# Performance work log

Hardware: AMD Instinct MI355X
Metric: run time of the kernel (lower is better)

Reference implementation:

```python
import jax, jax.numpy as jnp
import numpy as np

B, N, K = 8, 2048, 20  # clouds, points per cloud, kNN neighbors
NUM_CLASSES = 40


def _mlp3(x, w1, b1, w2, b2, w3, b3):
    x = jax.nn.relu(x @ w1 + b1)
    x = jax.nn.relu(x @ w2 + b2)
    return jax.nn.relu(x @ w3 + b3)


def _dynamic_edge_conv(x, w1, b1, w2, b2, w3, b3):
    # x: [B, N, D]. Recompute kNN graph in feature space (per cloud),
    # build edge features [x_i, x_j - x_i], MLP, max-aggregate over neighbors.
    s = jnp.sum(x * x, axis=-1)  # [B, N]
    d2 = s[:, :, None] + s[:, None, :] - 2.0 * jnp.einsum('bnd,bmd->bnm', x, x)  # [B,N,N]
    _, idx = jax.lax.top_k(-d2, K)  # [B, N, K], includes self (dist 0), matching torch_cluster.knn(x, x)
    xj = jax.vmap(lambda xb, ib: xb[ib])(x, idx)  # gather neighbors [B, N, K, D]
    xi = jnp.broadcast_to(x[:, :, None, :], xj.shape)
    e = jnp.concatenate([xi, xj - xi], axis=-1)  # [B, N, K, 2D]
    h = _mlp3(e, w1, b1, w2, b2, w3, b3)  # [B, N, K, H]
    return jnp.max(h, axis=2)  # max aggregation -> [B, N, H]


def setup_inputs() -> dict:
    key = jax.random.key(0)
    ks = jax.random.split(key, 32)

    def w(k, shape):
        fan_in = shape[0]
        return (jax.random.normal(k, shape, dtype=jnp.float32) / np.sqrt(fan_in)).astype(jnp.float32)

    inp = {
        'pos': jax.random.normal(ks[0], (B * N, 3), dtype=jnp.float32),
        'batch': jnp.repeat(jnp.arange(B, dtype=jnp.int64), N),
        # conv1 MLP: 6 -> 64 -> 64 -> 64
        'c1w1': w(ks[1], (6, 64)),   'c1b1': jnp.zeros((64,), jnp.float32),
        'c1w2': w(ks[2], (64, 64)),  'c1b2': jnp.zeros((64,), jnp.float32),
        'c1w3': w(ks[3], (64, 64)),  'c1b3': jnp.zeros((64,), jnp.float32),
        # conv2 MLP: 128 -> 128 -> 128 -> 256
        'c2w1': w(ks[4], (128, 128)), 'c2b1': jnp.zeros((128,), jnp.float32),
        'c2w2': w(ks[5], (128, 128)), 'c2b2': jnp.zeros((128,), jnp.float32),
        'c2w3': w(ks[6], (128, 256)), 'c2b3': jnp.zeros((256,), jnp.float32),
        # classifier head
        'l0w': w(ks[7], (256, 512)),  'l0b': jnp.zeros((512,), jnp.float32),
        'l1w': w(ks[8], (512, 256)),  'l1b': jnp.zeros((256,), jnp.float32),
        'l2w': w(ks[9], (256, 256)),  'l2b': jnp.zeros((256,), jnp.float32),
        'l3w': w(ks[10], (256, NUM_CLASSES)), 'l3b': jnp.zeros((NUM_CLASSES,), jnp.float32),
    }
    return inp


def reference(pos, batch,
              c1w1, c1b1, c1w2, c1b2, c1w3, c1b3,
              c2w1, c2b1, c2w2, c2b2, c2w3, c2b3,
              l0w, l0b, l1w, l1b, l2w, l2b, l3w, l3b):
    # batch is a contiguous equal-size partition: reshape to [B, N, 3]
    x = pos.reshape(B, N, 3)
    x = _dynamic_edge_conv(x, c1w1, c1b1, c1w2, c1b2, c1w3, c1b3)   # [B, N, 64]
    x = _dynamic_edge_conv(x, c2w1, c2b1, c2w2, c2b2, c2w3, c2b3)   # [B, N, 256]
    x = jax.nn.relu(x @ l0w + l0b)                                   # [B, N, 512]
    x = jnp.max(x, axis=1)                                           # global_max_pool -> [B, 512]
    x = jax.nn.relu(x @ l1w + l1b)
    x = jax.nn.relu(x @ l2w + l2b)
    # dropout(p=0.5) is identity at inference
    x = x @ l3w + l3b
    return jax.nn.log_softmax(x, axis=-1)  # [B, NUM_CLASSES]
```

## Files before the change

### kernel.cpp

```cpp
#include <hip/hip_runtime.h>
#include <hip/hip_bf16.h>
#include <math.h>

#define BB 8
#define NN 2048
#define KK 20

typedef short bf16x8 __attribute__((ext_vector_type(8)));
typedef float f32x4 __attribute__((ext_vector_type(4)));

__device__ __forceinline__ unsigned short f2bf(float f) {
  unsigned u = __float_as_uint(f);
  u += 0x7FFFu + ((u >> 16) & 1u);
  return (unsigned short)(u >> 16);
}
__device__ __forceinline__ float bf2f(unsigned short h) {
  return __uint_as_float(((unsigned)h) << 16);
}

__device__ __forceinline__ void topk_insert(float d, int m, float (&bd)[KK], int (&bi)[KK],
                                            float& worst, int& wslot) {
  if (d < worst) {
#pragma unroll
    for (int j = 0; j < KK; ++j) {
      if (j == wslot) { bd[j] = d; bi[j] = m; }
    }
    float w = -INFINITY;
    int s = 0;
#pragma unroll
    for (int j = 0; j < KK; ++j) {
      if (bd[j] > w) { w = bd[j]; s = j; }
    }
    worst = w;
    wslot = s;
  }
}

__device__ __forceinline__ void sins20(float (&s)[KK], float d) {
#pragma unroll
  for (int q = 0; q < KK - 1; ++q) s[q] = fminf(s[q], fmaxf(s[q + 1], d));
  s[KK - 1] = fminf(s[KK - 1], d);
}

__device__ __forceinline__ float knn1_dist(float sn, float ssq,
                                           float x0, float x1, float x2,
                                           float y0, float y1, float y2) {
  const float dot = fmaf(x0, y0, fmaf(x1, y1, x2 * y2));
  return fmaf(-2.f, dot, sn + ssq);
}

__global__ __launch_bounds__(256) void knn1_part(const float* __restrict__ pos,
                                                 float* __restrict__ candd,
                                                 int* __restrict__ candi) {
  __shared__ float xs0[256], xs1[256], xs2[256], ss[256];
  const int bid = blockIdx.x;
  const int b = bid >> 6;
  const int nc = (bid >> 3) & 7;
  const int mc = bid & 7;
  const int t = threadIdx.x;
  const float* posb = pos + (size_t)b * NN * 3;
  {
    const int m = mc * 256 + t;
    const float a0 = posb[m * 3 + 0];
    const float a1 = posb[m * 3 + 1];
    const float a2 = posb[m * 3 + 2];
    xs0[t] = a0; xs1[t] = a1; xs2[t] = a2;
    ss[t] = a0 * a0 + a1 * a1 + a2 * a2;
  }
  __syncthreads();
  const int n = nc * 256 + t;
  const float xn0 = posb[n * 3 + 0];
  const float xn1 = posb[n * 3 + 1];
  const float xn2 = posb[n * 3 + 2];
  const float sn = xn0 * xn0 + xn1 * xn1 + xn2 * xn2;

  float s[KK];
#pragma unroll
  for (int q = 0; q < KK; ++q) s[q] = INFINITY;
  for (int lm = 0; lm < 256; lm += 8) {
    float dv[8];
#pragma unroll
    for (int u = 0; u < 8; ++u)
      dv[u] = knn1_dist(sn, ss[lm + u], xn0, xn1, xn2, xs0[lm + u], xs1[lm + u], xs2[lm + u]);
#pragma unroll
    for (int u = 0; u < 8; ++u) sins20(s, dv[u]);
  }
  const float tau = s[0];

  int cA = 0;
  for (int lm = 0; lm < 256; lm += 8) {
#pragma unroll
    for (int u = 0; u < 8; ++u) {
      const float d = knn1_dist(sn, ss[lm + u], xn0, xn1, xn2, xs0[lm + u], xs1[lm + u], xs2[lm + u]);
      cA += (d < tau) ? 1 : 0;
    }
  }

  int posA = 0, posB = cA;
  const int rbase = mc * 256;
  const size_t obase = ((size_t)(b * 8 + mc) * KK) * 2048 + n;
  for (int lm = 0; lm < 256; lm += 8) {
#pragma unroll
    for (int u = 0; u < 8; ++u) {
      const float d = knn1_dist(sn, ss[lm + u], xn0, xn1, xn2, xs0[lm + u], xs1[lm + u], xs2[lm + u]);
      if (d < tau) {
        candd[obase + (size_t)posA * 2048] = d;
        candi[obase + (size_t)posA * 2048] = rbase + lm + u;
        ++posA;
      } else if (d == tau && posB < KK) {
        candd[obase + (size_t)posB * 2048] = d;
        candi[obase + (size_t)posB * 2048] = rbase + lm + u;
        ++posB;
      }
    }
  }
}

template <int NCH, int G>
__global__ __launch_bounds__(256) void merge_topk2(const float* __restrict__ candd,
                                                   const int* __restrict__ candi,
                                                   int* __restrict__ idx_out) {
  const int gid = blockIdx.x * 256 + threadIdx.x;
  const int pt = gid / G;
  const int sub = gid % G;
  const int b = pt >> 11, n = pt & 2047;
  constexpr int CPT = NCH / G;
  float bd[KK]; int bi[KK];
#pragma unroll
  for (int j = 0; j < KK; ++j) { bd[j] = INFINITY; bi[j] = 0; }
  float worst = INFINITY;
  int wslot = 0;
#pragma unroll
  for (int cc = 0; cc < CPT; ++cc) {
    const int c = sub * CPT + cc;
    const size_t base = ((size_t)(b * NCH + c) * KK) * 2048 + n;
    float dv[KK]; int iv[KK];
#pragma unroll
    for (int j = 0; j < KK; ++j) dv[j] = candd[base + (size_t)j * 2048];
#pragma unroll
    for (int j = 0; j < KK; ++j) iv[j] = candi[base + (size_t)j * 2048];
#pragma unroll
    for (int j = 0; j < KK; ++j) topk_insert(dv[j], iv[j], bd, bi, worst, wslot);
  }
#pragma unroll
  for (int stride = 1; stride < G; stride <<= 1) {
    float od[KK]; int oi[KK];
#pragma unroll
    for (int q = 0; q < KK; ++q) {
      od[q] = __shfl_xor(bd[q], stride);
      oi[q] = __shfl_xor(bi[q], stride);
    }
#pragma unroll
    for (int q = 0; q < KK; ++q) topk_insert(od[q], oi[q], bd, bi, worst, wslot);
  }
  if (sub == 0) {
    int* op = idx_out + (size_t)pt * KK;
#pragma unroll
    for (int j = 0; j < KK; ++j) op[j] = bi[j];
  }
}

__global__ __launch_bounds__(256) void pre1_kernel(const float* __restrict__ pos,
                                                   const float* __restrict__ w1,
                                                   const float* __restrict__ b1,
                                                   float* __restrict__ U1,
                                                   float* __restrict__ V1) {
  const int t = threadIdx.x;
  const int c = t & 63;
  const int n = blockIdx.x * 4 + (t >> 6);
  const float p0 = pos[(size_t)n * 3 + 0];
  const float p1 = pos[(size_t)n * 3 + 1];
  const float p2 = pos[(size_t)n * 3 + 2];
  const float wt0 = w1[0 * 64 + c], wt1 = w1[1 * 64 + c], wt2 = w1[2 * 64 + c];
  const float wb0 = w1[3 * 64 + c], wb1 = w1[4 * 64 + c], wb2 = w1[5 * 64 + c];
  float v = p0 * wb0 + p1 * wb1 + p2 * wb2;
  float u = p0 * (wt0 - wb0) + p1 * (wt1 - wb1) + p2 * (wt2 - wb2) + b1[c];
  U1[(size_t)n * 64 + c] = u;
  V1[(size_t)n * 64 + c] = v;
}

__global__ __launch_bounds__(256) void pre2_kernel(const float* __restrict__ x1,
                                                   const float* __restrict__ w1,
                                                   const float* __restrict__ b1,
                                                   float* __restrict__ U,
                                                   float* __restrict__ V) {
  __shared__ float X[64][68];
  const int nbase = blockIdx.x * 64;
  const int t = threadIdx.x;
  for (int it = t; it < 1024; it += 256) {
    const int r = it >> 4, q = it & 15;
    *(float4*)&X[r][q * 4] = *(const float4*)&x1[(size_t)(nbase + r) * 64 + q * 4];
  }
  __syncthreads();
  const int ty = t >> 4, tx = t & 15;
  const int c0 = tx * 8;
  float accT[4][8], accB[4][8];
#pragma unroll
  for (int u = 0; u < 4; ++u)
#pragma unroll
    for (int i = 0; i < 8; ++i) { accT[u][i] = 0.f; accB[u][i] = 0.f; }
  for (int d0 = 0; d0 < 64; d0 += 4) {
    float4 a[4];
#pragma unroll
    for (int u = 0; u < 4; ++u) a[u] = *(const float4*)&X[ty * 4 + u][d0];
#pragma unroll
    for (int dd = 0; dd < 4; ++dd) {
      const float4 t0 = *(const float4*)&w1[(size_t)(d0 + dd) * 128 + c0];
      const float4 t1 = *(const float4*)&w1[(size_t)(d0 + dd) * 128 + c0 + 4];
      const float4 bb0 = *(const float4*)&w1[(size_t)(64 + d0 + dd) * 128 + c0];
      const float4 bb1 = *(const float4*)&w1[(size_t)(64 + d0 + dd) * 128 + c0 + 4];
#pragma unroll
      for (int u = 0; u < 4; ++u) {
        const float av = (dd == 0) ? a[u].x : (dd == 1) ? a[u].y : (dd == 2) ? a[u].z : a[u].w;
        accT[u][0] = fmaf(av, t0.x, accT[u][0]);
        accT[u][1] = fmaf(av, t0.y, accT[u][1]);
        accT[u][2] = fmaf(av, t0.z, accT[u][2]);
        accT[u][3] = fmaf(av, t0.w, accT[u][3]);
        accT[u][4] = fmaf(av, t1.x, accT[u][4]);
        accT[u][5] = fmaf(av, t1.y, accT[u][5]);
        accT[u][6] = fmaf(av, t1.z, accT[u][6]);
        accT[u][7] = fmaf(av, t1.w, accT[u][7]);
        accB[u][0] = fmaf(av, bb0.x, accB[u][0]);
        accB[u][1] = fmaf(av, bb0.y, accB[u][1]);
        accB[u][2] = fmaf(av, bb0.z, accB[u][2]);
        accB[u][3] = fmaf(av, bb0.w, accB[u][3]);
        accB[u][4] = fmaf(av, bb1.x, accB[u][4]);
        accB[u][5] = fmaf(av, bb1.y, accB[u][5]);
        accB[u][6] = fmaf(av, bb1.z, accB[u][6]);
        accB[u][7] = fmaf(av, bb1.w, accB[u][7]);
      }
    }
  }
  const float4 bA = *(const float4*)&b1[c0];
  const float4 bB = *(const float4*)&b1[c0 + 4];
#pragma unroll
  for (int u = 0; u < 4; ++u) {
    const size_t row = (size_t)(nbase + ty * 4 + u) * 128 + c0;
    float4 u0, u1, v0, v1;
    v0 = make_float4(accB[u][0], accB[u][1], accB[u][2], accB[u][3]);
    v1 = make_float4(accB[u][4], accB[u][5], accB[u][6], accB[u][7]);
    u0.x = accT[u][0] - accB[u][0] + bA.x;
    u0.y = accT[u][1] - accB[u][1] + bA.y;
    u0.z = accT[u][2] - accB[u][2] + bA.z;
    u0.w = accT[u][3] - accB[u][3] + bA.w;
    u1.x = accT[u][4] - accB[u][4] + bB.x;
    u1.y = accT[u][5] - accB[u][5] + bB.y;
    u1.z = accT[u][6] - accB[u][6] + bB.z;
    u1.w = accT[u][7] - accB[u][7] + bB.w;
    *(float4*)&U[row] = u0;
    *(float4*)&U[row + 4] = u1;
    *(float4*)&V[row] = v0;
    *(float4*)&V[row + 4] = v1;
  }
}

__global__ __launch_bounds__(256) void wprep_kernel(
    const float* __restrict__ c2w2, const float* __restrict__ c2w3,
    const float* __restrict__ c1w2, const float* __restrict__ c1w3,
    unsigned short* __restrict__ w2t, unsigned short* __restrict__ w3t,
    unsigned short* __restrict__ c1w2hi, unsigned short* __restrict__ c1w2lo,
    unsigned short* __restrict__ c1w3hi, unsigned short* __restrict__ c1w3lo) {
  const int i = blockIdx.x * 256 + threadIdx.x;
  if (i < 16384) {
    const int d = i >> 7, c = i & 127;
    w2t[c * 128 + d] = f2bf(c2w2[i]);
  } else if (i < 49152) {
    const int j = i - 16384;
    const int d = j >> 8, c = j & 255;
    w3t[c * 128 + d] = f2bf(c2w3[j]);
  } else if (i < 53248) {
    const int j = i - 49152;
    const int d = j >> 6, c = j & 63;
    const float v = c1w2[j];
    const unsigned short h = f2bf(v);
    c1w2hi[c * 64 + d] = h;
    c1w2lo[c * 64 + d] = f2bf(v - bf2f(h));
  } else {
    const int j = i - 53248;
    const int d = j >> 6, c = j & 63;
    const float v = c1w3[j];
    const unsigned short h = f2bf(v);
    c1w3hi[c * 64 + d] = h;
    c1w3lo[c * 64 + d] = f2bf(v - bf2f(h));
  }
}

__global__ __launch_bounds__(256) void conv1_kernel(
    const float* __restrict__ U1, const float* __restrict__ V1,
    const int* __restrict__ idx,
    const unsigned short* __restrict__ w2hi, const unsigned short* __restrict__ w2lo,
    const float* __restrict__ b2,
    const unsigned short* __restrict__ w3hi, const unsigned short* __restrict__ w3lo,
    const float* __restrict__ b3,
    float* __restrict__ xout) {
  __shared__ __align__(16) unsigned short A[160][2][76];
  __shared__ unsigned int pm[8][64];
  const int bid = blockIdx.x;
  const int b = bid >> 8;
  const int pbase = (bid & 255) * 8;
  const int t = threadIdx.x;
  const int wave = t >> 6, lane = t & 63;
  const int lrow = lane & 15;
  const int lk8 = (lane >> 4) * 8;
  const int c = wave * 16 + lrow;

  for (int it = t; it < 2560; it += 256) {
    const int r = it >> 4, q = it & 15;
    const int p = r / 20, k = r - (r / 20) * 20;
    const int n = b * NN + pbase + p;
    const int j = b * NN + idx[(size_t)n * KK + k];
    const float4 uv = *(const float4*)&U1[(size_t)n * 64 + q * 4];
    const float4 vv = *(const float4*)&V1[(size_t)j * 64 + q * 4];
    float e[4];
    e[0] = fmaxf(uv.x + vv.x, 0.f);
    e[1] = fmaxf(uv.y + vv.y, 0.f);
    e[2] = fmaxf(uv.z + vv.z, 0.f);
    e[3] = fmaxf(uv.w + vv.w, 0.f);
    ushort4 hi, lo;
    hi.x = f2bf(e[0]); lo.x = f2bf(e[0] - bf2f(hi.x));
    hi.y = f2bf(e[1]); lo.y = f2bf(e[1] - bf2f(hi.y));
    hi.z = f2bf(e[2]); lo.z = f2bf(e[2] - bf2f(hi.z));
    hi.w = f2bf(e[3]); lo.w = f2bf(e[3] - bf2f(hi.w));
    *(ushort4*)&A[r][0][q * 4] = hi;
    *(ushort4*)&A[r][1][q * 4] = lo;
  }
  for (int i = t; i < 512; i += 256) ((unsigned int*)pm)[i] = 0u;
  __syncthreads();

  {
    bf16x8 whi[2], wlo[2];
#pragma unroll
    for (int ks = 0; ks < 2; ++ks) {
      whi[ks] = *(const bf16x8*)&w2hi[(size_t)c * 64 + ks * 32 + lk8];
      wlo[ks] = *(const bf16x8*)&w2lo[(size_t)c * 64 + ks * 32 + lk8];
    }
    f32x4 acc2[10];
#pragma unroll
    for (int mt = 0; mt < 10; ++mt) {
      bf16x8 ahi[2], alo[2];
#pragma unroll
      for (int ks = 0; ks < 2; ++ks) {
        ahi[ks] = *(const bf16x8*)&A[mt * 16 + lrow][0][ks * 32 + lk8];
        alo[ks] = *(const bf16x8*)&A[mt * 16 + lrow][1][ks * 32 + lk8];
      }
      f32x4 acc = {0.f, 0.f, 0.f, 0.f};
#pragma unroll
      for (int ks = 0; ks < 2; ++ks) {
        acc = __builtin_amdgcn_mfma_f32_16x16x32_bf16(ahi[ks], whi[ks], acc, 0, 0, 0);
        acc = __builtin_amdgcn_mfma_f32_16x16x32_bf16(ahi[ks], wlo[ks], acc, 0, 0, 0);
        acc = __builtin_amdgcn_mfma_f32_16x16x32_bf16(alo[ks], whi[ks], acc, 0, 0, 0);
      }
      acc2[mt] = acc;
    }
    __syncthreads();
    const float bias = b2[c];
#pragma unroll
    for (int mt = 0; mt < 10; ++mt) {
      const int r0 = mt * 16 + ((lane >> 4) << 2);
#pragma unroll
      for (int reg = 0; reg < 4; ++reg) {
        const float v = fmaxf(acc2[mt][reg] + bias, 0.f);
        const unsigned short h = f2bf(v);
        A[r0 + reg][0][c] = h;
        A[r0 + reg][1][c] = f2bf(v - bf2f(h));
      }
    }
  }
  __syncthreads();

  {
    bf16x8 whi[2], wlo[2];
#pragma unroll
    for (int ks = 0; ks < 2; ++ks) {
      whi[ks] = *(const bf16x8*)&w3hi[(size_t)c * 64 + ks * 32 + lk8];
      wlo[ks] = *(const bf16x8*)&w3lo[(size_t)c * 64 + ks * 32 + lk8];
    }
    const float bias = b3[c];
#pragma unroll
    for (int mt = 0; mt < 10; ++mt) {
      bf16x8 ahi[2], alo[2];
#pragma unroll
      for (int ks = 0; ks < 2; ++ks) {
        ahi[ks] = *(const bf16x8*)&A[mt * 16 + lrow][0][ks * 32 + lk8];
        alo[ks] = *(const bf16x8*)&A[mt * 16 + lrow][1][ks * 32 + lk8];
      }
      f32x4 acc = {0.f, 0.f, 0.f, 0.f};
#pragma unroll
      for (int ks = 0; ks < 2; ++ks) {
        acc = __builtin_amdgcn_mfma_f32_16x16x32_bf16(ahi[ks], whi[ks], acc, 0, 0, 0);
        acc = __builtin_amdgcn_mfma_f32_16x16x32_bf16(ahi[ks], wlo[ks], acc, 0, 0, 0);
        acc = __builtin_amdgcn_mfma_f32_16x16x32_bf16(alo[ks], whi[ks], acc, 0, 0, 0);
      }
      const int r0 = mt * 16 + ((lane >> 4) << 2);
      const float v0 = fmaxf(acc[0] + bias, 0.f);
      const float v1 = fmaxf(acc[1] + bias, 0.f);
      const float v2 = fmaxf(acc[2] + bias, 0.f);
      const float v3 = fmaxf(acc[3] + bias, 0.f);
      if (r0 / 20 == (r0 + 3) / 20) {
        atomicMax(&pm[r0 / 20][c], __float_as_uint(fmaxf(fmaxf(v0, v1), fmaxf(v2, v3))));
      } else {
        atomicMax(&pm[(r0 + 0) / 20][c], __float_as_uint(v0));
        atomicMax(&pm[(r0 + 1) / 20][c], __float_as_uint(v1));
        atomicMax(&pm[(r0 + 2) / 20][c], __float_as_uint(v2));
        atomicMax(&pm[(r0 + 3) / 20][c], __float_as_uint(v3));
      }
    }
  }
  __syncthreads();

  {
    const int p = t >> 5;
    const int cc = (t & 31) * 2;
    float2 o;
    o.x = __uint_as_float(pm[p][cc]);
    o.y = __uint_as_float(pm[p][cc + 1]);
    *(float2*)&xout[((size_t)(b * NN + pbase + p)) * 64 + cc] = o;
  }
}

__global__ __launch_bounds__(256) void xsplit_kernel(const float* __restrict__ x1,
                                                     unsigned short* __restrict__ xhi,
                                                     unsigned short* __restrict__ xlo,
                                                     float* __restrict__ s) {
  const int e = blockIdx.x * 256 + threadIdx.x;
  const int n = e >> 3, q = e & 7;
  const float4 v0 = *(const float4*)&x1[(size_t)n * 64 + q * 8];
  const float4 v1 = *(const float4*)&x1[(size_t)n * 64 + q * 8 + 4];
  float ps = v0.x * v0.x + v0.y * v0.y + v0.z * v0.z + v0.w * v0.w +
             v1.x * v1.x + v1.y * v1.y + v1.z * v1.z + v1.w * v1.w;
  ps += __shfl_xor(ps, 1);
  ps += __shfl_xor(ps, 2);
  ps += __shfl_xor(ps, 4);
  if (q == 0) s[n] = ps;
  const float vv[8] = {v0.x, v0.y, v0.z, v0.w, v1.x, v1.y, v1.z, v1.w};
  unsigned short hb[8], lb[8];
#pragma unroll
  for (int i = 0; i < 8; ++i) {
    hb[i] = f2bf(vv[i]);
    lb[i] = f2bf(vv[i] - bf2f(hb[i]));
  }
  *(ushort4*)&xhi[(size_t)n * 64 + q * 8] = make_ushort4(hb[0], hb[1], hb[2], hb[3]);
  *(ushort4*)&xhi[(size_t)n * 64 + q * 8 + 4] = make_ushort4(hb[4], hb[5], hb[6], hb[7]);
  *(ushort4*)&xlo[(size_t)n * 64 + q * 8] = make_ushort4(lb[0], lb[1], lb[2], lb[3]);
  *(ushort4*)&xlo[(size_t)n * 64 + q * 8 + 4] = make_ushort4(lb[4], lb[5], lb[6], lb[7]);
}

__global__ __launch_bounds__(256) void d2sel_kernel(const unsigned short* __restrict__ xhi,
                                                    const unsigned short* __restrict__ xlo,
                                                    const float* __restrict__ s,
                                                    float* __restrict__ candd,
                                                    int* __restrict__ candi) {
  __shared__ __align__(16) unsigned short SBUF[4 * 128 * 72];
  __shared__ float sA[128], sB[128];
  float (*Tt)[132] = (float(*)[132])SBUF;
  const int bid = blockIdx.x;
  const int b = bid >> 8;
  const int tile = bid & 255;
  const int ti = tile >> 4, tj = tile & 15;
  const int i0 = ti * 128, j0 = tj * 128;
  const int gb = b * NN;
  const int t = threadIdx.x;
  const int wave = t >> 6, lane = t & 63;
  const int lrow = lane & 15;
  const int lk8 = (lane >> 4) * 8;

  for (int it = t; it < 4096; it += 256) {
    const int part = it >> 10;
    const int r = (it >> 3) & 127;
    const int g = it & 7;
    const unsigned short* src = (part == 0) ? xhi : (part == 1) ? xlo
                               : (part == 2) ? xhi : xlo;
    const int base = (part < 2) ? i0 : j0;
    *(uint4*)&SBUF[part * 9216 + r * 72 + g * 8] =
        *(const uint4*)&src[((size_t)(gb + base + r)) * 64 + g * 8];
  }
  if (t < 128) sA[t] = s[gb + i0 + t];
  else sB[t - 128] = s[gb + j0 + (t - 128)];
  __syncthreads();

  bf16x8 ahi[2][2], alo[2][2];
#pragma unroll
  for (int mt = 0; mt < 2; ++mt) {
    const int r = wave * 32 + mt * 16 + lrow;
#pragma unroll
    for (int ks = 0; ks < 2; ++ks) {
      ahi[mt][ks] = *(const bf16x8*)&SBUF[0 * 9216 + r * 72 + ks * 32 + lk8];
      alo[mt][ks] = *(const bf16x8*)&SBUF[1 * 9216 + r * 72 + ks * 32 + lk8];
    }
  }
  f32x4 acc[2][8];
#pragma unroll
  for (int mt = 0; mt < 2; ++mt)
#pragma unroll
    for (int nt = 0; nt < 8; ++nt) acc[mt][nt] = (f32x4){0.f, 0.f, 0.f, 0.f};
#pragma unroll
  for (int nt = 0; nt < 8; ++nt) {
    bf16x8 bhi[2], blo[2];
#pragma unroll
    for (int ks = 0; ks < 2; ++ks) {
      bhi[ks] = *(const bf16x8*)&SBUF[2 * 9216 + (nt * 16 + lrow) * 72 + ks * 32 + lk8];
      blo[ks] = *(const bf16x8*)&SBUF[3 * 9216 + (nt * 16 + lrow) * 72 + ks * 32 + lk8];
    }
#pragma unroll
    for (int mt = 0; mt < 2; ++mt) {
#pragma unroll
      for (int ks = 0; ks < 2; ++ks) {
        acc[mt][nt] = __builtin_amdgcn_mfma_f32_16x16x32_bf16(ahi[mt][ks], bhi[ks], acc[mt][nt], 0, 0, 0);
        acc[mt][nt] = __builtin_amdgcn_mfma_f32_16x16x32_bf16(ahi[mt][ks], blo[ks], acc[mt][nt], 0, 0, 0);
        acc[mt][nt] = __builtin_amdgcn_mfma_f32_16x16x32_bf16(alo[mt][ks], bhi[ks], acc[mt][nt], 0, 0, 0);
      }
    }
  }
  __syncthreads();

#pragma unroll
  for (int mt = 0; mt < 2; ++mt) {
    const int ib = wave * 32 + mt * 16 + ((lane >> 4) << 2);
#pragma unroll
    for (int nt = 0; nt < 8; ++nt) {
      const int jj = nt * 16 + lrow;
      const float sj = sB[jj];
      float4 o;
      o.x = sA[ib + 0] + sj - 2.f * acc[mt][nt][0];
      o.y = sA[ib + 1] + sj - 2.f * acc[mt][nt][1];
      o.z = sA[ib + 2] + sj - 2.f * acc[mt][nt][2];
      o.w = sA[ib + 3] + sj - 2.f * acc[mt][nt][3];
      *(float4*)&Tt[jj][ib] = o;
    }
  }
  __syncthreads();

  const int j = t >> 1, h = t & 1;
  float sl[KK];
#pragma unroll
  for (int q = 0; q < KK; ++q) sl[q] = INFINITY;
  for (int r4 = 0; r4 < 16; ++r4) {
    const float4 v = *(const float4*)&Tt[j][h * 64 + r4 * 4];
    sins20(sl, v.x);
    sins20(sl, v.y);
    sins20(sl, v.z);
    sins20(sl, v.w);
  }
  {
    float od[KK];
#pragma unroll
    for (int q = 0; q < KK; ++q) od[q] = __shfl_xor(sl[q], 1);
#pragma unroll
    for (int q = 0; q < KK; ++q) sins20(sl, od[q]);
  }
  const float tau = sl[0];

  int cA = 0, cB = 0;
  for (int r4 = 0; r4 < 16; ++r4) {
    const float4 v = *(const float4*)&Tt[j][h * 64 + r4 * 4];
    cA += (v.x < tau) + (v.y < tau) + (v.z < tau) + (v.w < tau);
    cB += (v.x == tau) + (v.y == tau) + (v.z == tau) + (v.w == tau);
  }
  const int pA = __shfl_xor(cA, 1);
  const int pB = __shfl_xor(cB, 1);
  const int nA = cA + pA;
  int posA = h ? pA : 0;
  int posB = nA + (h ? pB : 0);

  const size_t obase = ((size_t)(b * 16 + ti) * KK) * 2048 + (j0 + j);
  for (int r4 = 0; r4 < 16; ++r4) {
    const float4 v = *(const float4*)&Tt[j][h * 64 + r4 * 4];
    const float dd[4] = {v.x, v.y, v.z, v.w};
#pragma unroll
    for (int u = 0; u < 4; ++u) {
      const float d = dd[u];
      const int row = i0 + h * 64 + r4 * 4 + u;
      if (d < tau) {
        candd[obase + (size_t)posA * 2048] = d;
        candi[obase + (size_t)posA * 2048] = row;
        ++posA;
      } else if (d == tau && posB < KK) {
        candd[obase + (size_t)posB * 2048] = d;
        candi[obase + (size_t)posB * 2048] = row;
        ++posB;
      }
    }
  }
}

__global__ __launch_bounds__(256) void conv2_kernel(
    const float* __restrict__ U, const float* __restrict__ V,
    const int* __restrict__ idx,
    const unsigned short* __restrict__ w2t, const float* __restrict__ b2,
    const unsigned short* __restrict__ w3t, const float* __restrict__ b3,
    float* __restrict__ xout) {
  __shared__ __align__(16) unsigned short E[80][136];
  __shared__ __align__(16) unsigned short E2[80][136];
  __shared__ unsigned int pm[4][256];
  const int bid = blockIdx.x;
  const int b = bid >> 9;
  const int pbase = (bid & 511) * 4;
  const int t = threadIdx.x;
  const int wave = t >> 6, lane = t & 63;
  const int lrow = lane & 15;
  const int lk8 = (lane >> 4) * 8;

  for (int it = t; it < 2560; it += 256) {
    const int r = it >> 5, q = it & 31;
    const int p = r / 20, k = r - (r / 20) * 20;
    const int n = b * NN + pbase + p;
    const int j = b * NN + idx[(size_t)n * KK + k];
    const float4 uv = *(const float4*)&U[(size_t)n * 128 + q * 4];
    const float4 vv = *(const float4*)&V[(size_t)j * 128 + q * 4];
    ushort4 h;
    h.x = f2bf(fmaxf(uv.x + vv.x, 0.f));
    h.y = f2bf(fmaxf(uv.y + vv.y, 0.f));
    h.z = f2bf(fmaxf(uv.z + vv.z, 0.f));
    h.w = f2bf(fmaxf(uv.w + vv.w, 0.f));
    *(ushort4*)&E[r][q * 4] = h;
  }
  for (int i = t; i < 1024; i += 256) ((unsigned int*)pm)[i] = 0u;
  __syncthreads();

  {
    bf16x8 wf[2][4];
#pragma unroll
    for (int nt2 = 0; nt2 < 2; ++nt2) {
      const int ntg = wave * 2 + nt2;
#pragma unroll
      for (int ks = 0; ks < 4; ++ks)
        wf[nt2][ks] = *(const bf16x8*)&w2t[(size_t)(ntg * 16 + lrow) * 128 + ks * 32 + lk8];
    }
    const float bias0 = b2[wave * 32 + lrow];
    const float bias1 = b2[wave * 32 + 16 + lrow];
#pragma unroll
    for (int mt = 0; mt < 5; ++mt) {
      bf16x8 af[4];
#pragma unroll
      for (int ks = 0; ks < 4; ++ks)
        af[ks] = *(const bf16x8*)&E[mt * 16 + lrow][ks * 32 + lk8];
      f32x4 acc0 = {0.f, 0.f, 0.f, 0.f};
      f32x4 acc1 = {0.f, 0.f, 0.f, 0.f};
#pragma unroll
      for (int ks = 0; ks < 4; ++ks) {
        acc0 = __builtin_amdgcn_mfma_f32_16x16x32_bf16(af[ks], wf[0][ks], acc0, 0, 0, 0);
        acc1 = __builtin_amdgcn_mfma_f32_16x16x32_bf16(af[ks], wf[1][ks], acc1, 0, 0, 0);
      }
      const int r0 = mt * 16 + ((lane >> 4) << 2);
      const int c0 = wave * 32 + lrow;
#pragma unroll
      for (int reg = 0; reg < 4; ++reg) {
        E2[r0 + reg][c0]      = f2bf(fmaxf(acc0[reg] + bias0, 0.f));
        E2[r0 + reg][c0 + 16] = f2bf(fmaxf(acc1[reg] + bias1, 0.f));
      }
    }
  }
  __syncthreads();

  {
    bf16x8 wf[4][4];
#pragma unroll
    for (int nt4 = 0; nt4 < 4; ++nt4) {
      const int ntg = wave * 4 + nt4;
#pragma unroll
      for (int ks = 0; ks < 4; ++ks)
        wf[nt4][ks] = *(const bf16x8*)&w3t[(size_t)(ntg * 16 + lrow) * 128 + ks * 32 + lk8];
    }
#pragma unroll
    for (int mt = 0; mt < 5; ++mt) {
      bf16x8 af[4];
#pragma unroll
      for (int ks = 0; ks < 4; ++ks)
        af[ks] = *(const bf16x8*)&E2[mt * 16 + lrow][ks * 32 + lk8];
      f32x4 acc[4];
#pragma unroll
      for (int nt4 = 0; nt4 < 4; ++nt4) acc[nt4] = (f32x4){0.f, 0.f, 0.f, 0.f};
#pragma unroll
      for (int ks = 0; ks < 4; ++ks) {
#pragma unroll
        for (int nt4 = 0; nt4 < 4; ++nt4)
          acc[nt4] = __builtin_amdgcn_mfma_f32_16x16x32_bf16(af[ks], wf[nt4][ks], acc[nt4], 0, 0, 0);
      }
      const int r0 = mt * 16 + ((lane >> 4) << 2);
      const int pa = r0 / 20;
      const int pb = (r0 + 3) / 20;
#pragma unroll
      for (int nt4 = 0; nt4 < 4; ++nt4) {
        const int c = wave * 64 + nt4 * 16 + lrow;
        const float bias = b3[c];
        float v0 = fmaxf(acc[nt4][0] + bias, 0.f);
        float v1 = fmaxf(acc[nt4][1] + bias, 0.f);
        float v2 = fmaxf(acc[nt4][2] + bias, 0.f);
        float v3 = fmaxf(acc[nt4][3] + bias, 0.f);
        if (pa == pb) {
          atomicMax(&pm[pa][c], __float_as_uint(fmaxf(fmaxf(v0, v1), fmaxf(v2, v3))));
        } else {
          atomicMax(&pm[(r0 + 0) / 20][c], __float_as_uint(v0));
          atomicMax(&pm[(r0 + 1) / 20][c], __float_as_uint(v1));
          atomicMax(&pm[(r0 + 2) / 20][c], __float_as_uint(v2));
          atomicMax(&pm[(r0 + 3) / 20][c], __float_as_uint(v3));
        }
      }
    }
  }
  __syncthreads();

  {
    const int p = t >> 6;
    const int c0 = (t & 63) * 4;
    const float4 o = *(const float4*)&pm[p][c0];
    *(float4*)&xout[((size_t)b * NN + pbase + p) * 256 + c0] = o;
  }
}

__global__ __launch_bounds__(256) void l0_kernel(const float* __restrict__ x2,
                                                 const float* __restrict__ w,
                                                 const float* __restrict__ bias,
                                                 float* __restrict__ gp) {
  __shared__ float A[64][68];
  __shared__ float red[16][128];
  const int bid = blockIdx.x;
  const int b = bid >> 7;
  const int mblk = (bid >> 2) & 31;
  const int cblk = bid & 3;
  const int t = threadIdx.x;
  const int ty = t >> 4, tx = t & 15;
  const float* xb = x2 + ((size_t)b * NN + mblk * 64) * 256;
  float acc[4][8];
#pragma unroll
  for (int u = 0; u < 4; ++u)
#pragma unroll
    for (int i = 0; i < 8; ++i) acc[u][i] = 0.f;
  for (int kc = 0; kc < 4; ++kc) {
    {
      const int r = t >> 2, seg = (t & 3) * 16;
#pragma unroll
      for (int s4 = 0; s4 < 4; ++s4) {
        *(float4*)&A[r][seg + s4 * 4] =
            *(const float4*)&xb[(size_t)r * 256 + kc * 64 + seg + s4 * 4];
      }
    }
    __syncthreads();
    for (int d0 = 0; d0 < 64; d0 += 4) {
      float4 a[4];
#pragma unroll
      for (int u = 0; u < 4; ++u) a[u] = *(const float4*)&A[ty * 4 + u][d0];
#pragma unroll
      for (int dd = 0; dd < 4; ++dd) {
        const size_t wrow = (size_t)(kc * 64 + d0 + dd) * 512 + cblk * 128 + tx * 8;
        const float4 wA = *(const float4*)&w[wrow];
        const float4 wB = *(const float4*)&w[wrow + 4];
#pragma unroll
        for (int u = 0; u < 4; ++u) {
          const float av = (dd == 0) ? a[u].x : (dd == 1) ? a[u].y : (dd == 2) ? a[u].z : a[u].w;
          acc[u][0] = fmaf(av, wA.x, acc[u][0]);
          acc[u][1] = fmaf(av, wA.y, acc[u][1]);
          acc[u][2] = fmaf(av, wA.z, acc[u][2]);
          acc[u][3] = fmaf(av, wA.w, acc[u][3]);
          acc[u][4] = fmaf(av, wB.x, acc[u][4]);
          acc[u][5] = fmaf(av, wB.y, acc[u][5]);
          acc[u][6] = fmaf(av, wB.z, acc[u][6]);
          acc[u][7] = fmaf(av, wB.w, acc[u][7]);
        }
      }
    }
    __syncthreads();
  }
  {
    float4 m0, m1;
    m0.x = fmaxf(fmaxf(acc[0][0], acc[1][0]), fmaxf(acc[2][0], acc[3][0]));
    m0.y = fmaxf(fmaxf(acc[0][1], acc[1][1]), fmaxf(acc[2][1], acc[3][1]));
    m0.z = fmaxf(fmaxf(acc[0][2], acc[1][2]), fmaxf(acc[2][2], acc[3][2]));
    m0.w = fmaxf(fmaxf(acc[0][3], acc[1][3]), fmaxf(acc[2][3], acc[3][3]));
    m1.x = fmaxf(fmaxf(acc[0][4], acc[1][4]), fmaxf(acc[2][4], acc[3][4]));
    m1.y = fmaxf(fmaxf(acc[0][5], acc[1][5]), fmaxf(acc[2][5], acc[3][5]));
    m1.z = fmaxf(fmaxf(acc[0][6], acc[1][6]), fmaxf(acc[2][6], acc[3][6]));
    m1.w = fmaxf(fmaxf(acc[0][7], acc[1][7]), fmaxf(acc[2][7], acc[3][7]));
    *(float4*)&red[ty][tx * 8] = m0;
    *(float4*)&red[ty][tx * 8 + 4] = m1;
  }
  __syncthreads();
  if (t < 128) {
    float m = red[0][t];
#pragma unroll
    for (int q = 1; q < 16; ++q) m = fmaxf(m, red[q][t]);
    m = fmaxf(m + bias[cblk * 128 + t], 0.f);
    gp[((size_t)b * 32 + mblk) * 512 + cblk * 128 + t] = m;
  }
}

__global__ __launch_bounds__(256) void head_kernel(
    const float* __restrict__ gp,
    const float* __restrict__ l1w, const float* __restrict__ l1b,
    const float* __restrict__ l2w, const float* __restrict__ l2b,
    const float* __restrict__ l3w, const float* __restrict__ l3b,
    float* __restrict__ out) {
  __shared__ float g[512];
  __shared__ float h1[256];
  __shared__ float h2[256];
  __shared__ float logits[40];
  __shared__ float lse_s;
  const int b = blockIdx.x;
  const int t = threadIdx.x;
  for (int cidx = t; cidx < 512; cidx += 256) {
    float m = gp[(size_t)(b * 32) * 512 + cidx];
    for (int ch = 1; ch < 32; ++ch) m = fmaxf(m, gp[(size_t)(b * 32 + ch) * 512 + cidx]);
    g[cidx] = m;
  }
  __syncthreads();
  {
    float acc = 0.f;
    for (int d = 0; d < 512; d += 4) {
      const float4 gv = *(const float4*)&g[d];
      acc = fmaf(gv.x, l1w[(size_t)d * 256 + t], acc);
      acc = fmaf(gv.y, l1w[(size_t)(d + 1) * 256 + t], acc);
      acc = fmaf(gv.z, l1w[(size_t)(d + 2) * 256 + t], acc);
      acc = fmaf(gv.w, l1w[(size_t)(d + 3) * 256 + t], acc);
    }
    h1[t] = fmaxf(acc + l1b[t], 0.f);
  }
  __syncthreads();
  {
    float acc = 0.f;
    for (int d = 0; d < 256; d += 4) {
      const float4 hv = *(const float4*)&h1[d];
      acc = fmaf(hv.x, l2w[(size_t)d * 256 + t], acc);
      acc = fmaf(hv.y, l2w[(size_t)(d + 1) * 256 + t], acc);
      acc = fmaf(hv.z, l2w[(size_t)(d + 2) * 256 + t], acc);
      acc = fmaf(hv.w, l2w[(size_t)(d + 3) * 256 + t], acc);
    }
    h2[t] = fmaxf(acc + l2b[t], 0.f);
  }
  __syncthreads();
  if (t < 40) {
    float acc = 0.f;
    for (int d = 0; d < 256; ++d) acc = fmaf(h2[d], l3w[(size_t)d * 40 + t], acc);
    logits[t] = acc + l3b[t];
  }
  __syncthreads();
  if (t == 0) {
    float M = -INFINITY;
    for (int j = 0; j < 40; ++j) M = fmaxf(M, logits[j]);
    float ssum = 0.f;
    for (int j = 0; j < 40; ++j) ssum += expf(logits[j] - M);
    lse_s = M + logf(ssum);
  }
  __syncthreads();
  if (t < 40) out[(size_t)b * 40 + t] = logits[t] - lse_s;
}

extern "C" void kernel_launch(void* const* d_in, const int* in_sizes, int n_in,
                              void* d_out, int out_size, void* d_ws, size_t ws_size,
                              hipStream_t stream) {
  const float* pos  = (const float*)d_in[0];
  const float* c1w1 = (const float*)d_in[2];
  const float* c1b1 = (const float*)d_in[3];
  const float* c1w2 = (const float*)d_in[4];
  const float* c1b2 = (const float*)d_in[5];
  const float* c1w3 = (const float*)d_in[6];
  const float* c1b3 = (const float*)d_in[7];
  const float* c2w1 = (const float*)d_in[8];
  const float* c2b1 = (const float*)d_in[9];
  const float* c2w2 = (const float*)d_in[10];
  const float* c2b2 = (const float*)d_in[11];
  const float* c2w3 = (const float*)d_in[12];
  const float* c2b3 = (const float*)d_in[13];
  const float* l0w  = (const float*)d_in[14];
  const float* l0b  = (const float*)d_in[15];
  const float* l1w  = (const float*)d_in[16];
  const float* l1b  = (const float*)d_in[17];
  const float* l2w  = (const float*)d_in[18];
  const float* l2b  = (const float*)d_in[19];
  const float* l3w  = (const float*)d_in[20];
  const float* l3b  = (const float*)d_in[21];
  float* out = (float*)d_out;

  char* ws = (char*)d_ws;
  float* x1    = (float*)(ws + 0);
  float* x2    = (float*)(ws + ((size_t)4 << 20));
  int*   idx1  = (int*)  (ws + ((size_t)20 << 20));
  int*   idx2  = (int*)  (ws + ((size_t)22 << 20));
  float* gp    = (float*)(ws + ((size_t)24 << 20));
  unsigned short* w2t    = (unsigned short*)(ws + ((size_t)24 << 20) + (512 << 10));
  unsigned short* w3t    = (unsigned short*)(ws + ((size_t)24 << 20) + (544 << 10));
  unsigned short* c1w2hi = (unsigned short*)(ws + ((size_t)24 << 20) + (608 << 10));
  unsigned short* c1w2lo = (unsigned short*)(ws + ((size_t)24 << 20) + (616 << 10));
  unsigned short* c1w3hi = (unsigned short*)(ws + ((size_t)24 << 20) + (624 << 10));
  unsigned short* c1w3lo = (unsigned short*)(ws + ((size_t)24 << 20) + (632 << 10));
  float* candd = (float*)(ws + ((size_t)25 << 20));
  int*   candi = (int*)  (ws + ((size_t)46 << 20));
  float* U1 = (float*)(ws + ((size_t)25 << 20));
  float* V1 = (float*)(ws + ((size_t)29 << 20));
  float* U  = (float*)(ws + ((size_t)46 << 20));
  float* Vv = (float*)(ws + ((size_t)54 << 20));
  unsigned short* xhi = (unsigned short*)(ws + ((size_t)62 << 20));
  unsigned short* xlo = (unsigned short*)(ws + ((size_t)64 << 20));
  float* sbuf = (float*)(ws + ((size_t)66 << 20));

  wprep_kernel<<<224, 256, 0, stream>>>(c2w2, c2w3, c1w2, c1w3,
                                        w2t, w3t, c1w2hi, c1w2lo, c1w3hi, c1w3lo);
  knn1_part<<<512, 256, 0, stream>>>(pos, candd, candi);
  merge_topk2<8, 4><<<256, 256, 0, stream>>>(candd, candi, idx1);
  pre1_kernel<<<4096, 256, 0, stream>>>(pos, c1w1, c1b1, U1, V1);
  conv1_kernel<<<2048, 256, 0, stream>>>(U1, V1, idx1, c1w2hi, c1w2lo, c1b2,
                                         c1w3hi, c1w3lo, c1b3, x1);
  xsplit_kernel<<<512, 256, 0, stream>>>(x1, xhi, xlo, sbuf);
  d2sel_kernel<<<2048, 256, 0, stream>>>(xhi, xlo, sbuf, candd, candi);
  merge_topk2<16, 8><<<512, 256, 0, stream>>>(candd, candi, idx2);
  pre2_kernel<<<256, 256, 0, stream>>>(x1, c2w1, c2b1, U, Vv);
  conv2_kernel<<<4096, 256, 0, stream>>>(U, Vv, idx2, w2t, c2b2, w3t, c2b3, x2);
  l0_kernel<<<1024, 256, 0, stream>>>(x2, l0w, l0b, gp);
  head_kernel<<<8, 256, 0, stream>>>(gp, l1w, l1b, l2w, l2b, l3w, l3b, out);
}
```

Measured before the change: 552.9 us.

## Move l0 layer to split-bf16 MFMA and reuse conv2 LDS buffer

The l0 linear layer moves from scalar FP32 FMAs to bf16 MFMA using a hi/lo split (three MFMAs per product) to keep near-fp32 accuracy. Its weights are transposed and split in wprep, and conv2 now writes x2 as hi/lo bf16 pairs. Conv2 also drops its second LDS buffer by holding layer-2 accumulators in registers across a barrier and writing them back into E, which cuts shared memory to allow more resident blocks. The cost is extra register pressure in conv2 and a larger weight-prep kernel.

After: 492.5 us. 10.9% less time.

```diff
diff --git a/kernel.cpp b/kernel.cpp
--- a/kernel.cpp
+++ b/kernel.cpp
@@ -257,9 +257,11 @@
 __global__ __launch_bounds__(256) void wprep_kernel(
     const float* __restrict__ c2w2, const float* __restrict__ c2w3,
     const float* __restrict__ c1w2, const float* __restrict__ c1w3,
+    const float* __restrict__ l0w,
     unsigned short* __restrict__ w2t, unsigned short* __restrict__ w3t,
     unsigned short* __restrict__ c1w2hi, unsigned short* __restrict__ c1w2lo,
-    unsigned short* __restrict__ c1w3hi, unsigned short* __restrict__ c1w3lo) {
+    unsigned short* __restrict__ c1w3hi, unsigned short* __restrict__ c1w3lo,
+    unsigned short* __restrict__ l0thi, unsigned short* __restrict__ l0tlo) {
   const int i = blockIdx.x * 256 + threadIdx.x;
   if (i < 16384) {
     const int d = i >> 7, c = i & 127;
@@ -275,13 +277,20 @@
     const unsigned short h = f2bf(v);
     c1w2hi[c * 64 + d] = h;
     c1w2lo[c * 64 + d] = f2bf(v - bf2f(h));
-  } else {
+  } else if (i < 57344) {
     const int j = i - 53248;
     const int d = j >> 6, c = j & 63;
     const float v = c1w3[j];
     const unsigned short h = f2bf(v);
     c1w3hi[c * 64 + d] = h;
     c1w3lo[c * 64 + d] = f2bf(v - bf2f(h));
+  } else if (i < 188416) {
+    const int j = i - 57344;
+    const int d = j >> 9, c = j & 511;
+    const float v = l0w[j];
+    const unsigned short h = f2bf(v);
+    l0thi[c * 256 + d] = h;
+    l0tlo[c * 256 + d] = f2bf(v - bf2f(h));
   }
 }
 
@@ -588,9 +597,8 @@
     const int* __restrict__ idx,
     const unsigned short* __restrict__ w2t, const float* __restrict__ b2,
     const unsigned short* __restrict__ w3t, const float* __restrict__ b3,
-    float* __restrict__ xout) {
+    unsigned short* __restrict__ x2hi, unsigned short* __restrict__ x2lo) {
   __shared__ __align__(16) unsigned short E[80][136];
-  __shared__ __align__(16) unsigned short E2[80][136];
   __shared__ unsigned int pm[4][256];
   const int bid = blockIdx.x;
   const int b = bid >> 9;
@@ -626,8 +634,7 @@
       for (int ks = 0; ks < 4; ++ks)
         wf[nt2][ks] = *(const bf16x8*)&w2t[(size_t)(ntg * 16 + lrow) * 128 + ks * 32 + lk8];
     }
-    const float bias0 = b2[wave * 32 + lrow];
-    const float bias1 = b2[wave * 32 + 16 + lrow];
+    f32x4 a0buf[5], a1buf[5];
 #pragma unroll
     for (int mt = 0; mt < 5; ++mt) {
       bf16x8 af[4];
@@ -641,12 +648,20 @@
         acc0 = __builtin_amdgcn_mfma_f32_16x16x32_bf16(af[ks], wf[0][ks], acc0, 0, 0, 0);
         acc1 = __builtin_amdgcn_mfma_f32_16x16x32_bf16(af[ks], wf[1][ks], acc1, 0, 0, 0);
       }
+      a0buf[mt] = acc0;
+      a1buf[mt] = acc1;
+    }
+    __syncthreads();
+    const float bias0 = b2[wave * 32 + lrow];
+    const float bias1 = b2[wave * 32 + 16 + lrow];
+#pragma unroll
+    for (int mt = 0; mt < 5; ++mt) {
       const int r0 = mt * 16 + ((lane >> 4) << 2);
       const int c0 = wave * 32 + lrow;
 #pragma unroll
       for (int reg = 0; reg < 4; ++reg) {
-        E2[r0 + reg][c0]      = f2bf(fmaxf(acc0[reg] + bias0, 0.f));
-        E2[r0 + reg][c0 + 16] = f2bf(fmaxf(acc1[reg] + bias1, 0.f));
+        E[r0 + reg][c0]      = f2bf(fmaxf(a0buf[mt][reg] + bias0, 0.f));
+        E[r0 + reg][c0 + 16] = f2bf(fmaxf(a1buf[mt][reg] + bias1, 0.f));
       }
     }
   }
@@ -666,7 +681,7 @@
       bf16x8 af[4];
 #pragma unroll
       for (int ks = 0; ks < 4; ++ks)
-        af[ks] = *(const bf16x8*)&E2[mt * 16 + lrow][ks * 32 + lk8];
+        af[ks] = *(const bf16x8*)&E[mt * 16 + lrow][ks * 32 + lk8];
       f32x4 acc[4];
 #pragma unroll
       for (int nt4 = 0; nt4 < 4; ++nt4) acc[nt4] = (f32x4){0.f, 0.f, 0.f, 0.f};
@@ -704,84 +719,100 @@
     const int p = t >> 6;
     const int c0 = (t & 63) * 4;
     const float4 o = *(const float4*)&pm[p][c0];
-    *(float4*)&xout[((size_t)b * NN + pbase + p) * 256 + c0] = o;
-  }
-}
-
-__global__ __launch_bounds__(256) void l0_kernel(const float* __restrict__ x2,
-                                                 const float* __restrict__ w,
-                                                 const float* __restrict__ bias,
-                                                 float* __restrict__ gp) {
-  __shared__ float A[64][68];
-  __shared__ float red[16][128];
+    ushort4 hi, lo;
+    hi.x = f2bf(o.x); lo.x = f2bf(o.x - bf2f(hi.x));
+    hi.y = f2bf(o.y); lo.y = f2bf(o.y - bf2f(hi.y));
+    hi.z = f2bf(o.z); lo.z = f2bf(o.z - bf2f(hi.z));
+    hi.w = f2bf(o.w); lo.w = f2bf(o.w - bf2f(hi.w));
+    const size_t base = ((size_t)b * NN + pbase + p) * 256 + c0;
+    *(ushort4*)&x2hi[base] = hi;
+    *(ushort4*)&x2lo[base] = lo;
+  }
+}
+
+__global__ __launch_bounds__(256) void l0_kernel(
+    const unsigned short* __restrict__ x2hi, const unsigned short* __restrict__ x2lo,
+    const unsigned short* __restrict__ l0thi, const unsigned short* __restrict__ l0tlo,
+    const float* __restrict__ bias, float* __restrict__ gp) {
+  __shared__ __align__(16) unsigned short Ahi[64][72];
+  __shared__ __align__(16) unsigned short Alo[64][72];
+  __shared__ unsigned int pm[256];
   const int bid = blockIdx.x;
-  const int b = bid >> 7;
-  const int mblk = (bid >> 2) & 31;
-  const int cblk = bid & 3;
+  const int cblk = bid & 1;
+  const int mblk = (bid >> 1) & 31;
+  const int b = bid >> 6;
   const int t = threadIdx.x;
-  const int ty = t >> 4, tx = t & 15;
-  const float* xb = x2 + ((size_t)b * NN + mblk * 64) * 256;
-  float acc[4][8];
-#pragma unroll
-  for (int u = 0; u < 4; ++u)
-#pragma unroll
-    for (int i = 0; i < 8; ++i) acc[u][i] = 0.f;
+  const int wave = t >> 6, lane = t & 63;
+  const int lrow = lane & 15;
+  const int lk8 = (lane >> 4) * 8;
+  const size_t rowbase = (size_t)(b * NN + mblk * 64);
+  const int cbase = cblk * 256;
+
+  pm[t] = 0u;
+
+  f32x4 acc[4][4];
+#pragma unroll
+  for (int mt = 0; mt < 4; ++mt)
+#pragma unroll
+    for (int nt = 0; nt < 4; ++nt) acc[mt][nt] = (f32x4){0.f, 0.f, 0.f, 0.f};
+
   for (int kc = 0; kc < 4; ++kc) {
-    {
-      const int r = t >> 2, seg = (t & 3) * 16;
-#pragma unroll
-      for (int s4 = 0; s4 < 4; ++s4) {
-        *(float4*)&A[r][seg + s4 * 4] =
-            *(const float4*)&xb[(size_t)r * 256 + kc * 64 + seg + s4 * 4];
-      }
+    for (int it = t; it < 1024; it += 256) {
+      const int buf = it >> 9;
+      const int r = (it >> 3) & 63;
+      const int g = it & 7;
+      const unsigned short* src = buf ? x2lo : x2hi;
+      const uint4 v = *(const uint4*)&src[(rowbase + r) * 256 + kc * 64 + g * 8];
+      if (buf) *(uint4*)&Alo[r][g * 8] = v;
+      else     *(uint4*)&Ahi[r][g * 8] = v;
     }
     __syncthreads();
-    for (int d0 = 0; d0 < 64; d0 += 4) {
-      float4 a[4];
-#pragma unroll
-      for (int u = 0; u < 4; ++u) a[u] = *(const float4*)&A[ty * 4 + u][d0];
-#pragma unroll
-      for (int dd = 0; dd < 4; ++dd) {
-        const size_t wrow = (size_t)(kc * 64 + d0 + dd) * 512 + cblk * 128 + tx * 8;
-        const float4 wA = *(const float4*)&w[wrow];
-        const float4 wB = *(const float4*)&w[wrow + 4];
-#pragma unroll
-        for (int u = 0; u < 4; ++u) {
-          const float av = (dd == 0) ? a[u].x : (dd == 1) ? a[u].y : (dd == 2) ? a[u].z : a[u].w;
-          acc[u][0] = fmaf(av, wA.x, acc[u][0]);
-          acc[u][1] = fmaf(av, wA.y, acc[u][1]);
-          acc[u][2] = fmaf(av, wA.z, acc[u][2]);
-          acc[u][3] = fmaf(av, wA.w, acc[u][3]);
-          acc[u][4] = fmaf(av, wB.x, acc[u][4]);
-          acc[u][5] = fmaf(av, wB.y, acc[u][5]);
-          acc[u][6] = fmaf(av, wB.z, acc[u][6]);
-          acc[u][7] = fmaf(av, wB.w, acc[u][7]);
+
+    bf16x8 bhi[4][2], blo[4][2];
+#pragma unroll
+    for (int nt = 0; nt < 4; ++nt) {
+      const size_t c = (size_t)(cbase + wave * 64 + nt * 16 + lrow);
+#pragma unroll
+      for (int ks = 0; ks < 2; ++ks) {
+        bhi[nt][ks] = *(const bf16x8*)&l0thi[c * 256 + kc * 64 + ks * 32 + lk8];
+        blo[nt][ks] = *(const bf16x8*)&l0tlo[c * 256 + kc * 64 + ks * 32 + lk8];
+      }
+    }
+#pragma unroll
+    for (int mt = 0; mt < 4; ++mt) {
+      bf16x8 ahi[2], alo[2];
+#pragma unroll
+      for (int ks = 0; ks < 2; ++ks) {
+        ahi[ks] = *(const bf16x8*)&Ahi[mt * 16 + lrow][ks * 32 + lk8];
+        alo[ks] = *(const bf16x8*)&Alo[mt * 16 + lrow][ks * 32 + lk8];
+      }
+#pragma unroll
+      for (int nt = 0; nt < 4; ++nt) {
+#pragma unroll
+        for (int ks = 0; ks < 2; ++ks) {
+          acc[mt][nt] = __builtin_amdgcn_mfma_f32_16x16x32_bf16(ahi[ks], bhi[nt][ks], acc[mt][nt], 0, 0, 0);
+          acc[mt][nt] = __builtin_amdgcn_mfma_f32_16x16x32_bf16(ahi[ks], blo[nt][ks], acc[mt][nt], 0, 0, 0);
+          acc[mt][nt] = __builtin_amdgcn_mfma_f32_16x16x32_bf16(alo[ks], bhi[nt][ks], acc[mt][nt], 0, 0, 0);
         }
       }
     }
     __syncthreads();
   }
-  {
-    float4 m0, m1;
-    m0.x = fmaxf(fmaxf(acc[0][0], acc[1][0]), fmaxf(acc[2][0], acc[3][0]));
-    m0.y = fmaxf(fmaxf(acc[0][1], acc[1][1]), fmaxf(acc[2][1], acc[3][1]));
-    m0.z = fmaxf(fmaxf(acc[0][2], acc[1][2]), fmaxf(acc[2][2], acc[3][2]));
-    m0.w = fmaxf(fmaxf(acc[0][3], acc[1][3]), fmaxf(acc[2][3], acc[3][3]));
-    m1.x = fmaxf(fmaxf(acc[0][4], acc[1][4]), fmaxf(acc[2][4], acc[3][4]));
-    m1.y = fmaxf(fmaxf(acc[0][5], acc[1][5]), fmaxf(acc[2][5], acc[3][5]));
-    m1.z = fmaxf(fmaxf(acc[0][6], acc[1][6]), fmaxf(acc[2][6], acc[3][6]));
-    m1.w = fmaxf(fmaxf(acc[0][7], acc[1][7]), fmaxf(acc[2][7], acc[3][7]));
-    *(float4*)&red[ty][tx * 8] = m0;
-    *(float4*)&red[ty][tx * 8 + 4] = m1;
-  }
-  __syncthreads();
-  if (t < 128) {
-    float m = red[0][t];
-#pragma unroll
-    for (int q = 1; q < 16; ++q) m = fmaxf(m, red[q][t]);
-    m = fmaxf(m + bias[cblk * 128 + t], 0.f);
-    gp[((size_t)b * 32 + mblk) * 512 + cblk * 128 + t] = m;
-  }
+
+#pragma unroll
+  for (int nt = 0; nt < 4; ++nt) {
+    const int cl = wave * 64 + nt * 16 + lrow;
+    const float bv = bias[cbase + cl];
+    float mx = 0.f;
+#pragma unroll
+    for (int mt = 0; mt < 4; ++mt)
+#pragma unroll
+      for (int reg = 0; reg < 4; ++reg)
+        mx = fmaxf(mx, fmaxf(acc[mt][nt][reg] + bv, 0.f));
+    atomicMax(&pm[cl], __float_as_uint(mx));
+  }
+  __syncthreads();
+  gp[((size_t)(b * 32 + mblk)) * 512 + cbase + t] = __uint_as_float(pm[t]);
 }
 
 __global__ __launch_bounds__(256) void head_kernel(
@@ -872,7 +903,6 @@
 
   char* ws = (char*)d_ws;
   float* x1    = (float*)(ws + 0);
-  float* x2    = (float*)(ws + ((size_t)4 << 20));
   int*   idx1  = (int*)  (ws + ((size_t)20 << 20));
   int*   idx2  = (int*)  (ws + ((size_t)22 << 20));
   float* gp    = (float*)(ws + ((size_t)24 << 20));
@@ -888,12 +918,17 @@
   float* V1 = (float*)(ws + ((size_t)29 << 20));
   float* U  = (float*)(ws + ((size_t)46 << 20));
   float* Vv = (float*)(ws + ((size_t)54 << 20));
-  unsigned short* xhi = (unsigned short*)(ws + ((size_t)62 << 20));
-  unsigned short* xlo = (unsigned short*)(ws + ((size_t)64 << 20));
-  float* sbuf = (float*)(ws + ((size_t)66 << 20));
-
-  wprep_kernel<<<224, 256, 0, stream>>>(c2w2, c2w3, c1w2, c1w3,
-                                        w2t, w3t, c1w2hi, c1w2lo, c1w3hi, c1w3lo);
+  unsigned short* xhi  = (unsigned short*)(ws + ((size_t)68 << 20));
+  unsigned short* xlo  = (unsigned short*)(ws + ((size_t)70 << 20));
+  float*          sbuf = (float*)         (ws + ((size_t)72 << 20));
+  unsigned short* x2hi = (unsigned short*)(ws + ((size_t)73 << 20));
+  unsigned short* x2lo = (unsigned short*)(ws + ((size_t)81 << 20));
+  unsigned short* l0thi = (unsigned short*)(ws + ((size_t)89 << 20));
+  unsigned short* l0tlo = (unsigned short*)(ws + ((size_t)89 << 20) + (256 << 10));
+
+  wprep_kernel<<<736, 256, 0, stream>>>(c2w2, c2w3, c1w2, c1w3, l0w,
+                                        w2t, w3t, c1w2hi, c1w2lo, c1w3hi, c1w3lo,
+                                        l0thi, l0tlo);
   knn1_part<<<512, 256, 0, stream>>>(pos, candd, candi);
   merge_topk2<8, 4><<<256, 256, 0, stream>>>(candd, candi, idx1);
   pre1_kernel<<<4096, 256, 0, stream>>>(pos, c1w1, c1b1, U1, V1);
@@ -903,7 +938,7 @@
   d2sel_kernel<<<2048, 256, 0, stream>>>(xhi, xlo, sbuf, candd, candi);
   merge_topk2<16, 8><<<512, 256, 0, stream>>>(candd, candi, idx2);
   pre2_kernel<<<256, 256, 0, stream>>>(x1, c2w1, c2b1, U, Vv);
-  conv2_kernel<<<4096, 256, 0, stream>>>(U, Vv, idx2, w2t, c2b2, w3t, c2b3, x2);
-  l0_kernel<<<1024, 256, 0, stream>>>(x2, l0w, l0b, gp);
+  conv2_kernel<<<4096, 256, 0, stream>>>(U, Vv, idx2, w2t, c2b2, w3t, c2b3, x2hi, x2lo);
+  l0_kernel<<<512, 256, 0, stream>>>(x2hi, x2lo, l0thi, l0tlo, l0b, gp);
   head_kernel<<<8, 256, 0, stream>>>(gp, l1w, l1b, l2w, l2b, l3w, l3b, out);
 }
```
